# Optimization experiments

Measured on AMD Instinct MI355X. Metric: run time of the kernel, lower is better.

The kernel has to match this reference:

```python
import jax, jax.numpy as jnp
import numpy as np

DIMS, HEAD, FREQ = 1024, 16, 10000
HEAD_DIM = DIMS // HEAD          # 64
ROT = HEAD_DIM // 2              # 32
B, S = 4, 8192


def setup_inputs() -> dict:
    key = jax.random.key(0)
    k1, k2, k3, k4 = jax.random.split(key, 4)
    x = jax.random.normal(k1, (B, S, DIMS), dtype=jnp.float32)
    matrix = jax.random.normal(k2, (HEAD_DIM, HEAD_DIM), dtype=jnp.float32)
    thetas = jax.random.normal(k3, (ROT,), dtype=jnp.float32) * 0.1
    tscale = jnp.ones((1,), dtype=jnp.float32)
    # inverse frequencies exactly as in __init__
    invf = (1.0 / FREQ ** (jnp.arange(0, HEAD_DIM, 2, dtype=jnp.float32) / HEAD_DIM)).astype(jnp.float32)
    pairs = jax.random.randint(k4, (ROT, 2), 0, HEAD_DIM, dtype=jnp.int32)
    return {"x": x, "matrix": matrix, "thetas": thetas, "tscale": tscale,
            "invf": invf, "pairs": pairs}


def _composed_rotation(thetas, tscale, pairs, d, dtype):
    # Build every Givens matrix G_k (same element-set order as the torch code)
    theta = thetas * tscale[0]

    def make_G(i, j, th):
        c, sn = jnp.cos(th), jnp.sin(th)
        G = jnp.eye(d, dtype=dtype)
        return G.at[i, i].set(c).at[j, j].set(c).at[i, j].set(-sn).at[j, i].set(sn)

    Gs = jax.vmap(make_G)(pairs[:, 0], pairs[:, 1], theta)  # [rot, d, d]

    def step(acc, G):
        return acc @ G, None

    G_comb, _ = jax.lax.scan(step, jnp.eye(d, dtype=dtype), Gs)
    return G_comb


def reference(x, matrix, thetas, tscale, invf, pairs):
    b, s, dims = x.shape
    d = matrix.shape[0]          # head_dim
    h = dims // d                # heads

    G_comb = _composed_rotation(thetas, tscale, pairs, d, x.dtype)

    xr = x.reshape(b, s, h, d)
    # flat @ G_combined @ self.matrix (acts on last dim)
    xr = xr @ (G_comb @ matrix)

    # sinusoidal RoPE: sinusoid[s, d/2] = pos * invf
    pos = jnp.arange(s, dtype=x.dtype)
    sinusoid = pos[:, None] * invf[None, :]
    sin = jnp.sin(sinusoid)[None, :, None, :]   # [1, s, 1, d/2]
    cos = jnp.cos(sinusoid)[None, :, None, :]

    x1, x2 = xr[..., ::2], xr[..., 1::2]
    out = jnp.concatenate([x1 * cos - x2 * sin, x1 * sin + x2 * cos], axis=-1)
    return out.reshape(b, s, dims) * jnp.asarray(np.sqrt(dims), x.dtype)
```

## Files before the change

### kernel.cpp

```cpp
#include <hip/hip_runtime.h>
#include <math.h>

#define BB 4
#define SS 8192
#define HH 16
#define DD 64
#define ROT 32
#define NG (BB * SS * HH)
#define TPB 256
#define TILES 2
#define NBLK (NG / (16 * 4 * TILES))
#define LSTR 65

typedef float f32x4 __attribute__((ext_vector_type(4)));
typedef float f32x2 __attribute__((ext_vector_type(2)));
typedef short bf16x8 __attribute__((ext_vector_type(8)));

__global__ void setup_GM(const float* __restrict__ thetas,
                         const float* __restrict__ tscale,
                         const int* __restrict__ pairs,
                         const float* __restrict__ matrix,
                         float* __restrict__ M,
                         unsigned short* __restrict__ Mhi,
                         unsigned short* __restrict__ Mlo) {
  __shared__ float Gs[DD][DD];
  const int t = threadIdx.x;
  if (t < DD) {
    for (int c = 0; c < DD; ++c) Gs[t][c] = (t == c) ? 1.0f : 0.0f;
    const float ts = tscale[0];
    for (int r = 0; r < ROT; ++r) {
      const int i = pairs[2 * r], j = pairs[2 * r + 1];
      const float th = thetas[r] * ts;
      const float cc = cosf(th), sn = sinf(th);
      if (i == j) {
        Gs[t][i] *= sn;
      } else {
        const float a = Gs[t][i], b = Gs[t][j];
        Gs[t][i] = a * cc + b * sn;
        Gs[t][j] = b * cc - a * sn;
      }
    }
  }
  __syncthreads();
  const int e = blockIdx.x * 256 + t;
  const int k = e >> 6, col = e & 63;
  float a0 = 0.f, a1 = 0.f, a2 = 0.f, a3 = 0.f;
  for (int kk = 0; kk < DD; kk += 4) {
    a0 = fmaf(Gs[k][kk], matrix[kk * DD + col], a0);
    a1 = fmaf(Gs[k][kk + 1], matrix[(kk + 1) * DD + col], a1);
    a2 = fmaf(Gs[k][kk + 2], matrix[(kk + 2) * DD + col], a2);
    a3 = fmaf(Gs[k][kk + 3], matrix[(kk + 3) * DD + col], a3);
  }
  const float val = (a0 + a1) + (a2 + a3);
  M[e] = val;

  const int G = col & 3;
  const int v = col >> 2;
  const int lane = ((k >> 3) & 3) * 16 + v;
  const int f = G * 2 + (k >> 5);
  const int idx = (f * 64 + lane) * 8 + (k & 7);
  const unsigned int b = __float_as_uint(val);
  const unsigned int hb = b & 0xFFFF0000u;
  const float rem = val - __uint_as_float(hb);
  Mhi[idx] = (unsigned short)(b >> 16);
  Mlo[idx] = (unsigned short)(__float_as_uint(rem) >> 16);
}

__global__ void setup_tab2(const float* __restrict__ invf,
                           float* __restrict__ tab2) {
  const int idx = blockIdx.x * 256 + threadIdx.x;
  if (idx >= SS * 16) return;
  const int s = idx >> 4, v = idx & 15;
  const float a0 = (float)s * invf[2 * v];
  const float a1 = (float)s * invf[2 * v + 1];
  float4 t;
  t.x = 32.0f * cosf(a0);
  t.y = 32.0f * sinf(a0);
  t.z = 32.0f * cosf(a1);
  t.w = 32.0f * sinf(a1);
  ((float4*)tab2)[idx] = t;
}

__device__ __forceinline__ unsigned int pack_hi(float u, float v, float& ru,
                                                float& rv) {
  const unsigned int bu = __float_as_uint(u);
  const unsigned int bv = __float_as_uint(v);
  const unsigned int hv = bv & 0xFFFF0000u;
  ru = u - __uint_as_float(bu & 0xFFFF0000u);
  rv = v - __uint_as_float(hv);
  return (bu >> 16) | hv;
}
__device__ __forceinline__ unsigned int pack_lo(float ru, float rv) {
  return (__float_as_uint(ru) >> 16) | (__float_as_uint(rv) & 0xFFFF0000u);
}
__device__ __forceinline__ void cvt8(const f32x4 a, const f32x4 b, bf16x8& hi,
                                     bf16x8& lo) {
  unsigned int* hp = (unsigned int*)&hi;
  unsigned int* lp = (unsigned int*)&lo;
  float r0, r1;
  hp[0] = pack_hi(a[0], a[1], r0, r1);
  lp[0] = pack_lo(r0, r1);
  hp[1] = pack_hi(a[2], a[3], r0, r1);
  lp[1] = pack_lo(r0, r1);
  hp[2] = pack_hi(b[0], b[1], r0, r1);
  lp[2] = pack_lo(r0, r1);
  hp[3] = pack_hi(b[2], b[3], r0, r1);
  lp[3] = pack_lo(r0, r1);
}

__device__ __forceinline__ void proc_token(
    const f32x4 c0, const f32x4 c1, const f32x4 c2, const f32x4 c3,
    const f32x4 tv, const bf16x8* bh, const bf16x8* bl,
    float* __restrict__ og, const int lk, const int l15) {
  bf16x8 ah0, al0, ah1, al1;
  cvt8(c0, c1, ah0, al0);
  cvt8(c2, c3, ah1, al1);
  f32x4 acc[4];
#pragma unroll
  for (int G = 0; G < 4; ++G) {
    f32x4 a_ = {0.f, 0.f, 0.f, 0.f};
    a_ = __builtin_amdgcn_mfma_f32_16x16x32_bf16(ah0, bh[2 * G], a_, 0, 0, 0);
    a_ = __builtin_amdgcn_mfma_f32_16x16x32_bf16(ah1, bh[2 * G + 1], a_, 0, 0, 0);
    a_ = __builtin_amdgcn_mfma_f32_16x16x32_bf16(ah0, bl[2 * G], a_, 0, 0, 0);
    a_ = __builtin_amdgcn_mfma_f32_16x16x32_bf16(ah1, bl[2 * G + 1], a_, 0, 0, 0);
    a_ = __builtin_amdgcn_mfma_f32_16x16x32_bf16(al0, bh[2 * G], a_, 0, 0, 0);
    a_ = __builtin_amdgcn_mfma_f32_16x16x32_bf16(al1, bh[2 * G + 1], a_, 0, 0, 0);
    acc[G] = a_;
  }
  const float cz0 = tv[0], sz0 = tv[1], cz1 = tv[2], sz1 = tv[3];
#pragma unroll
  for (int q = 0; q < 4; ++q) {
    const float e0 = acc[0][q], o0 = acc[1][q];
    const float e1 = acc[2][q], o1 = acc[3][q];
    f32x2 lo, hi;
    lo[0] = fmaf(e0, cz0, -(o0 * sz0));
    lo[1] = fmaf(e1, cz1, -(o1 * sz1));
    hi[0] = fmaf(e0, sz0, o0 * cz0);
    hi[1] = fmaf(e1, sz1, o1 * cz1);
    const int ro = (lk * 4 + q) * DD + 2 * l15;
    *(f32x2*)(og + ro) = lo;
    *(f32x2*)(og + ro + 32) = hi;
  }
}

__global__ __launch_bounds__(TPB, 3) void apply_rot(
    const float* __restrict__ x, const unsigned short* __restrict__ Mhi,
    const unsigned short* __restrict__ Mlo, const float* __restrict__ tab2,
    float* __restrict__ out) {
  const int tid = threadIdx.x;
  const int w = tid >> 6;
  const int l = tid & 63;
  const int l15 = l & 15, lk = l >> 4;

  bf16x8 bh[8], bl[8];
#pragma unroll
  for (int f = 0; f < 8; ++f) {
    bh[f] = *(const bf16x8*)(Mhi + (f * 64 + l) * 8);
    bl[f] = *(const bf16x8*)(Mlo + (f * 64 + l) * 8);
  }

  const size_t tok0 = (size_t)blockIdx.x * 8 + w;
  const size_t tok1 = tok0 + 4;
  const float* __restrict__ xp0 = x + (tok0 * 16 + l15) * DD + lk * 8;
  const float* __restrict__ xp1 = x + (tok1 * 16 + l15) * DD + lk * 8;

  const f32x4 a0 = *(const f32x4*)(xp0);
  const f32x4 a1 = *(const f32x4*)(xp0 + 4);
  const f32x4 a2 = *(const f32x4*)(xp0 + 32);
  const f32x4 a3 = *(const f32x4*)(xp0 + 36);
  const int sp0 = (int)(tok0 & (SS - 1));
  const f32x4 tv0 = *(const f32x4*)(tab2 + (size_t)sp0 * 64 + l15 * 4);
  const f32x4 b0 = *(const f32x4*)(xp1);
  const f32x4 b1 = *(const f32x4*)(xp1 + 4);
  const f32x4 b2 = *(const f32x4*)(xp1 + 32);
  const f32x4 b3 = *(const f32x4*)(xp1 + 36);
  const int sp1 = (int)(tok1 & (SS - 1));
  const f32x4 tv1 = *(const f32x4*)(tab2 + (size_t)sp1 * 64 + l15 * 4);

  proc_token(a0, a1, a2, a3, tv0, bh, bl, out + tok0 * 16 * DD, lk, l15);
  proc_token(b0, b1, b2, b3, tv1, bh, bl, out + tok1 * 16 * DD, lk, l15);
}

__global__ __launch_bounds__(256, 8) void apply_rot_fb(
    const float* __restrict__ x, const float* __restrict__ M,
    const float* __restrict__ invf, float* __restrict__ out) {
  __shared__ float lds[64 * LSTR];
  const int tid = threadIdx.x;
  const size_t R0 = (size_t)blockIdx.x * 64;
  const float4* __restrict__ xg = (const float4*)x + R0 * 16;
#pragma unroll
  for (int i = 0; i < 4; ++i) {
    const int f = i * 256 + tid;
    *(float4*)&lds[(f >> 4) * LSTR + (f & 15) * 4] = xg[f];
  }
  __syncthreads();
  const int r = tid & 63;
  const int h = __builtin_amdgcn_readfirstlane(tid >> 6);
  const float* __restrict__ Mh = M + h * 16;
  const float* __restrict__ xr = &lds[r * LSTR];
  float acc[16];
#pragma unroll
  for (int c = 0; c < 16; ++c) acc[c] = 0.0f;
#pragma unroll 4
  for (int k4 = 0; k4 < 16; ++k4) {
    const float4 xv = *(const float4*)&xr[k4 * 4];
    const float* __restrict__ m0 = Mh + k4 * 4 * DD;
#pragma unroll
    for (int c = 0; c < 16; ++c) acc[c] = fmaf(xv.x, m0[c], acc[c]);
#pragma unroll
    for (int c = 0; c < 16; ++c) acc[c] = fmaf(xv.y, m0[DD + c], acc[c]);
#pragma unroll
    for (int c = 0; c < 16; ++c) acc[c] = fmaf(xv.z, m0[2 * DD + c], acc[c]);
#pragma unroll
    for (int c = 0; c < 16; ++c) acc[c] = fmaf(xv.w, m0[3 * DD + c], acc[c]);
  }
  const int g = (int)R0 + r;
  const int spos = (g >> 4) & (SS - 1);
  float cz[8], sz[8];
#pragma unroll
  for (int d = 0; d < 8; ++d) {
    const float ang = (float)spos * invf[h * 8 + d];
    cz[d] = 32.0f * cosf(ang);
    sz[d] = 32.0f * sinf(ang);
  }
  float4 lov[2], hiv[2];
#pragma unroll
  for (int q = 0; q < 2; ++q) {
#pragma unroll
    for (int d = 0; d < 4; ++d) {
      const int dd = 4 * q + d;
      const float e = acc[2 * dd], o = acc[2 * dd + 1];
      ((float*)&lov[q])[d] = e * cz[dd] - o * sz[dd];
      ((float*)&hiv[q])[d] = e * sz[dd] + o * cz[dd];
    }
  }
  __syncthreads();
  float* __restrict__ orow = &lds[r * LSTR];
  *(float4*)&orow[8 * h + 0] = lov[0];
  *(float4*)&orow[8 * h + 4] = lov[1];
  *(float4*)&orow[32 + 8 * h + 0] = hiv[0];
  *(float4*)&orow[32 + 8 * h + 4] = hiv[1];
  __syncthreads();
  float4* __restrict__ og = (float4*)out + R0 * 16;
#pragma unroll
  for (int i = 0; i < 4; ++i) {
    const int f = i * 256 + tid;
    og[f] = *(float4*)&lds[(f >> 4) * LSTR + (f & 15) * 4];
  }
}

extern "C" void kernel_launch(void* const* d_in, const int* in_sizes, int n_in,
                              void* d_out, int out_size, void* d_ws,
                              size_t ws_size, hipStream_t stream) {
  const float* x = (const float*)d_in[0];
  const float* matrix = (const float*)d_in[1];
  const float* thetas = (const float*)d_in[2];
  const float* tscale = (const float*)d_in[3];
  const float* invf = (const float*)d_in[4];
  const int* pairs = (const int*)d_in[5];
  float* out = (float*)d_out;

  float* M = (float*)d_ws;
  unsigned short* Mhi = (unsigned short*)(M + DD * DD);
  unsigned short* Mlo = Mhi + DD * DD;
  float* tab2 = (float*)(Mlo + DD * DD);
  const size_t need =
      (size_t)DD * DD * 4 + (size_t)DD * DD * 4 + (size_t)SS * 64 * 4;
  const bool have_tab = ws_size >= need;

  setup_GM<<<16, 256, 0, stream>>>(thetas, tscale, pairs, matrix, M, Mhi, Mlo);
  if (have_tab) {
    setup_tab2<<<(SS * 16) / 256, 256, 0, stream>>>(invf, tab2);
    apply_rot<<<NBLK, TPB, 0, stream>>>(x, Mhi, Mlo, tab2, out);
  } else {
    apply_rot_fb<<<NG / 64, 256, 0, stream>>>(x, M, invf, out);
  }
}
```

Before: 255.1 us.

## Make apply_rot persistent per wave with double-buffered token prefetch

Each wave now processes 16 consecutive tokens in a loop instead of two, prefetching the inputs and sin/cos table entries for token t+2 while computing token t. The goal is to amortize the per-block load of the split-bf16 matrix fragments and to hide global memory latency with software pipelining. In exchange the block count drops eightfold and launch bounds fall from 3 to 2 blocks per CU, which reduces occupancy and may leave fewer waves to hide latency on a memory-bound kernel.

Result: slower. 264.9 us (+3.8%).

```diff
diff --git a/kernel.cpp b/kernel.cpp
--- a/kernel.cpp
+++ b/kernel.cpp
@@ -7,9 +7,10 @@
 #define DD 64
 #define ROT 32
 #define NG (BB * SS * HH)
+#define NTOK (NG / HH)
 #define TPB 256
-#define TILES 2
-#define NBLK (NG / (16 * 4 * TILES))
+#define TPW 16
+#define NBLK (NTOK / (4 * TPW))
 #define LSTR 65
 
 typedef float f32x4 __attribute__((ext_vector_type(4)));
@@ -143,7 +144,7 @@
   }
 }
 
-__global__ __launch_bounds__(TPB, 3) void apply_rot(
+__global__ __launch_bounds__(TPB, 2) void apply_rot(
     const float* __restrict__ x, const unsigned short* __restrict__ Mhi,
     const unsigned short* __restrict__ Mlo, const float* __restrict__ tab2,
     float* __restrict__ out) {
@@ -159,26 +160,76 @@
     bl[f] = *(const bf16x8*)(Mlo + (f * 64 + l) * 8);
   }
 
-  const size_t tok0 = (size_t)blockIdx.x * 8 + w;
-  const size_t tok1 = tok0 + 4;
-  const float* __restrict__ xp0 = x + (tok0 * 16 + l15) * DD + lk * 8;
-  const float* __restrict__ xp1 = x + (tok1 * 16 + l15) * DD + lk * 8;
-
-  const f32x4 a0 = *(const f32x4*)(xp0);
-  const f32x4 a1 = *(const f32x4*)(xp0 + 4);
-  const f32x4 a2 = *(const f32x4*)(xp0 + 32);
-  const f32x4 a3 = *(const f32x4*)(xp0 + 36);
+  const size_t tok0 = ((size_t)blockIdx.x * 4 + w) * TPW;
+  const float* __restrict__ xp = x + (tok0 * 16 + l15) * DD + lk * 8;
+  float* __restrict__ op = out + tok0 * 16 * DD;
   const int sp0 = (int)(tok0 & (SS - 1));
-  const f32x4 tv0 = *(const f32x4*)(tab2 + (size_t)sp0 * 64 + l15 * 4);
-  const f32x4 b0 = *(const f32x4*)(xp1);
-  const f32x4 b1 = *(const f32x4*)(xp1 + 4);
-  const f32x4 b2 = *(const f32x4*)(xp1 + 32);
-  const f32x4 b3 = *(const f32x4*)(xp1 + 36);
-  const int sp1 = (int)(tok1 & (SS - 1));
-  const f32x4 tv1 = *(const f32x4*)(tab2 + (size_t)sp1 * 64 + l15 * 4);
-
-  proc_token(a0, a1, a2, a3, tv0, bh, bl, out + tok0 * 16 * DD, lk, l15);
-  proc_token(b0, b1, b2, b3, tv1, bh, bl, out + tok1 * 16 * DD, lk, l15);
+
+  f32x4 a0 = *(const f32x4*)(xp);
+  f32x4 a1 = *(const f32x4*)(xp + 4);
+  f32x4 a2 = *(const f32x4*)(xp + 32);
+  f32x4 a3 = *(const f32x4*)(xp + 36);
+  f32x4 tva = *(const f32x4*)(tab2 + (size_t)sp0 * 64 + l15 * 4);
+  const float* __restrict__ xq = xp + 16 * DD;
+  f32x4 b0 = *(const f32x4*)(xq);
+  f32x4 b1 = *(const f32x4*)(xq + 4);
+  f32x4 b2 = *(const f32x4*)(xq + 32);
+  f32x4 b3 = *(const f32x4*)(xq + 36);
+  f32x4 tvb = *(const f32x4*)(tab2 + (size_t)(sp0 + 1) * 64 + l15 * 4);
+
+#define PROC(C0, C1, C2, C3, TV, T)                                          \
+  {                                                                          \
+    bf16x8 ah0, al0, ah1, al1;                                               \
+    cvt8(C0, C1, ah0, al0);                                                  \
+    cvt8(C2, C3, ah1, al1);                                                  \
+    const f32x4 tv_ = TV;                                                    \
+    if ((T) + 2 < TPW) {           \
+      const float* __restrict__ p = xp + (size_t)((T) + 2) * 16 * DD;        \
+      C0 = *(const f32x4*)(p);                                               \
+      C1 = *(const f32x4*)(p + 4);                                           \
+      C2 = *(const f32x4*)(p + 32);                                          \
+      C3 = *(const f32x4*)(p + 36);                                          \
+      TV = *(const f32x4*)(tab2 + (size_t)(sp0 + (T) + 2) * 64 + l15 * 4);   \
+    }                                                                        \
+    f32x4 acc[4];                                                            \
+    _Pragma("unroll") for (int G = 0; G < 4; ++G) {                          \
+      f32x4 a_ = {0.f, 0.f, 0.f, 0.f};                                       \
+      a_ = __builtin_amdgcn_mfma_f32_16x16x32_bf16(ah0, bh[2 * G], a_, 0, 0, \
+                                                   0);                       \
+      a_ = __builtin_amdgcn_mfma_f32_16x16x32_bf16(ah1, bh[2 * G + 1], a_,   \
+                                                   0, 0, 0);                 \
+      a_ = __builtin_amdgcn_mfma_f32_16x16x32_bf16(ah0, bl[2 * G], a_, 0, 0, \
+                                                   0);                       \
+      a_ = __builtin_amdgcn_mfma_f32_16x16x32_bf16(ah1, bl[2 * G + 1], a_,   \
+                                                   0, 0, 0);                 \
+      a_ = __builtin_amdgcn_mfma_f32_16x16x32_bf16(al0, bh[2 * G], a_, 0, 0, \
+                                                   0);                       \
+      a_ = __builtin_amdgcn_mfma_f32_16x16x32_bf16(al1, bh[2 * G + 1], a_,   \
+                                                   0, 0, 0);                 \
+      acc[G] = a_;                                                           \
+    }                                                                        \
+    float* __restrict__ og = op + (size_t)(T) * 16 * DD;                     \
+    const float cz0 = tv_[0], sz0 = tv_[1], cz1 = tv_[2], sz1 = tv_[3];      \
+    _Pragma("unroll") for (int q = 0; q < 4; ++q) {                          \
+      const float e0 = acc[0][q], o0 = acc[1][q];                            \
+      const float e1 = acc[2][q], o1 = acc[3][q];                            \
+      f32x2 lo, hi;                                                          \
+      lo[0] = fmaf(e0, cz0, -(o0 * sz0));                                    \
+      lo[1] = fmaf(e1, cz1, -(o1 * sz1));                                    \
+      hi[0] = fmaf(e0, sz0, o0 * cz0);                                       \
+      hi[1] = fmaf(e1, sz1, o1 * cz1);                                       \
+      const int ro = (lk * 4 + q) * DD + 2 * l15;                            \
+      *(f32x2*)(og + ro) = lo;                                               \
+      *(f32x2*)(og + ro + 32) = hi;                                          \
+    }                                                                        \
+  }
+
+#pragma unroll 1
+  for (int t = 0; t < TPW; t += 2) {
+    PROC(a0, a1, a2, a3, tva, t);
+    PROC(b0, b1, b2, b3, tvb, t + 1);
+  }
+#undef PROC
 }
 
 __global__ __launch_bounds__(256, 8) void apply_rot_fb(
```
